# Performance work log

Hardware: AMD Instinct MI355X
Metric: run time of the kernel (lower is better)

The kernel has to match this reference:

```python
import jax, jax.numpy as jnp
import numpy as np

B, L, CIN, C = 256, 65, 2053, 512
SCALE = 1.0 / float(np.sqrt(C))


def _attn_layer(x, Wq, bq, Wk, bk, Wv, bv):
    # x: [B, Cin, L]; Conv1d(kernel=1) == channel-mixing matmul
    q = jnp.einsum('oi,bil->bol', Wq, x) + bq[:, None]
    k = jnp.einsum('oi,bil->bol', Wk, x) + bk[:, None]
    v = jax.nn.leaky_relu(jnp.einsum('oi,bil->bol', Wv, x) + bv[:, None], 0.01)
    # att[b,l,m] = <q[:,l], k[:,m]> / sqrt(C); softmax over m
    att = jax.nn.softmax(jnp.einsum('bcl,bcm->blm', q, k) * SCALE, axis=-1)
    # original: sum_m att[b,l,1,m] * v[b,1,c,m] -> [B,L,C] -> permute -> [B,C,L]
    out = jnp.einsum('blm,bcm->bcl', att, v)
    return out + x if out.shape == x.shape else out  # residual only when channels match


def _transform(x, Wq0, bq0, Wk0, bk0, Wv0, bv0, Wq, bq, Wk, bk, Wv, bv):
    x = _attn_layer(x, Wq0, bq0, Wk0, bk0, Wv0, bv0)
    for n in range(3):  # layers 1..3, C->C with residual
        x = _attn_layer(x, Wq[n], bq[n], Wk[n], bk[n], Wv[n], bv[n])
    return x


def setup_inputs():
    key = jax.random.key(0)
    ks = jax.random.split(key, 20)
    s = 0.02
    inp = {
        'dataleft': jax.random.normal(ks[0], (B, L, CIN), jnp.float32),
        'dataright': jax.random.normal(ks[1], (B, L, CIN), jnp.float32),
        # layer-0 QKV conv1d (k=1) weights: [C, CIN]
        'Wq0': jax.random.normal(ks[2], (C, CIN), jnp.float32) * s,
        'bq0': jnp.zeros((C,), jnp.float32),
        'Wk0': jax.random.normal(ks[3], (C, CIN), jnp.float32) * s,
        'bk0': jnp.zeros((C,), jnp.float32),
        'Wv0': jax.random.normal(ks[4], (C, CIN), jnp.float32) * s,
        'bv0': jnp.zeros((C,), jnp.float32),
        # layers 1..3 stacked: [3, C, C]
        'Wq': jax.random.normal(ks[5], (3, C, C), jnp.float32) * s,
        'bq': jnp.zeros((3, C), jnp.float32),
        'Wk': jax.random.normal(ks[6], (3, C, C), jnp.float32) * s,
        'bk': jnp.zeros((3, C), jnp.float32),
        'Wv': jax.random.normal(ks[7], (3, C, C), jnp.float32) * s,
        'bv': jnp.zeros((3, C), jnp.float32),
        # classifier: fc1(1024->256), fc2(256->2)
        'W1': jax.random.normal(ks[8], (256, 2 * C), jnp.float32) * s,
        'b1': jnp.zeros((256,), jnp.float32),
        'W2': jax.random.normal(ks[9], (2, 256), jnp.float32) * s,
        'b2': jnp.zeros((2,), jnp.float32),
    }
    return inp


def reference(dataleft, dataright, Wq0, bq0, Wk0, bk0, Wv0, bv0,
              Wq, bq, Wk, bk, Wv, bv, W1, b1, W2, b2):
    xl = jnp.transpose(dataleft, (0, 2, 1))   # [B, CIN, L]
    xr = jnp.transpose(dataright, (0, 2, 1))
    xl = _transform(xl, Wq0, bq0, Wk0, bk0, Wv0, bv0, Wq, bq, Wk, bk, Wv, bv)
    xr = _transform(xr, Wq0, bq0, Wk0, bk0, Wv0, bv0, Wq, bq, Wk, bk, Wv, bv)
    # AdaptiveAvgPool2d((512,1)) on [B,512,L]: identity over channel dim, mean over L
    xl = jnp.mean(xl, axis=-1)  # [B, C]
    xr = jnp.mean(xr, axis=-1)
    h = jnp.concatenate([xl, xr], axis=1)            # [B, 2C]
    h = jax.nn.relu(h @ W1.T + b1)                   # [B, 256]
    y = h @ W2.T + b2                                # [B, 2]
    return y  # training mode: no final softmax
```

## Files before the change

kernel.cpp:

```cpp
#include <hip/hip_runtime.h>
#include <hip/hip_bf16.h>

#define BF16 __hip_bfloat16

typedef __bf16 bf16x8 __attribute__((ext_vector_type(8)));
typedef float f32x4 __attribute__((ext_vector_type(4)));

__device__ __forceinline__ void async_copy16(const void* g, void* l) {
    __builtin_amdgcn_global_load_lds(
        (const __attribute__((address_space(1))) void*)g,
        (__attribute__((address_space(3))) void*)l,
        16, 0, 0);
}

__global__ __launch_bounds__(256) void convert_pad_k(
    const float* __restrict__ src, BF16* __restrict__ dst,
    long pairs, int Ks, int Kd) {
    long p = (long)blockIdx.x * blockDim.x + threadIdx.x;
    if (p >= pairs) return;
    long e = p * 2;
    long r = e / Kd;
    int k = (int)(e - r * Kd);
    float a = (k < Ks) ? src[r * Ks + k] : 0.f;
    float b = (k + 1 < Ks) ? src[r * Ks + k + 1] : 0.f;
    dst[e] = __float2bfloat16(a);
    dst[e + 1] = __float2bfloat16(b);
}

__global__ __launch_bounds__(256, 3) void gemm_qkv(
    const BF16* __restrict__ Xg, const BF16* __restrict__ Wg,
    const float* __restrict__ bqp, const float* __restrict__ bkp, const float* __restrict__ bvp,
    BF16* __restrict__ Qo, BF16* __restrict__ Ko, BF16* __restrict__ Vo,
    int K, int vtmode) {
    __shared__ __align__(16) BF16 Xs[2][128 * 32];
    __shared__ __align__(16) BF16 Ws[2][128 * 32];
    const int tid = threadIdx.x;
    const int w = tid >> 6;
    const int lane = tid & 63;
    const int quad = lane >> 4;
    const int l15 = lane & 15;
    const long n0 = (long)blockIdx.y * 128;
    const int m0full = blockIdx.x * 128;
    const int sel = blockIdx.x >> 2;
    const int mbase = (blockIdx.x & 3) * 128;
    const int wn = (w & 1) * 64;
    const int wm = (w >> 1) * 64;
    const int srow = lane >> 2;
    const int skoff = (lane & 3) * 8;
    f32x4 acc[4][4] = {};
    for (int k0 = 0; k0 < K; k0 += 64) {
#pragma unroll
        for (int sub = 0; sub < 2; ++sub) {
#pragma unroll
            for (int c = 0; c < 2; ++c) {
                const int rbase = w * 32 + c * 16;
                const int kcol = k0 + sub * 32 + skoff;
                async_copy16(Xg + (n0 + rbase + srow) * K + kcol, &Xs[sub][rbase * 32]);
                async_copy16(Wg + (long)(m0full + rbase + srow) * K + kcol, &Ws[sub][rbase * 32]);
            }
        }
        __syncthreads();
#pragma unroll
        for (int sub = 0; sub < 2; ++sub) {
            bf16x8 af[4], bfr[4];
#pragma unroll
            for (int i = 0; i < 4; ++i)
                af[i] = *(const bf16x8*)&Xs[sub][(wn + i * 16 + l15) * 32 + quad * 8];
#pragma unroll
            for (int j = 0; j < 4; ++j)
                bfr[j] = *(const bf16x8*)&Ws[sub][(wm + j * 16 + l15) * 32 + quad * 8];
#pragma unroll
            for (int i = 0; i < 4; ++i)
#pragma unroll
                for (int j = 0; j < 4; ++j)
                    acc[i][j] = __builtin_amdgcn_mfma_f32_16x16x32_bf16(af[i], bfr[j], acc[i][j], 0, 0, 0);
        }
        __syncthreads();
    }
    const float* bp = (sel == 0) ? bqp : (sel == 1) ? bkp : bvp;
    BF16* out = (sel == 0) ? Qo : (sel == 1) ? Ko : Vo;
#pragma unroll
    for (int j = 0; j < 4; ++j) {
        const int m = mbase + wm + j * 16 + l15;
        const float bz = bp[m];
#pragma unroll
        for (int i = 0; i < 4; ++i) {
#pragma unroll
            for (int r = 0; r < 4; ++r) {
                const long n = n0 + wn + i * 16 + quad * 4 + r;
                float v = acc[i][j][r] + bz;
                if (sel == 2) {
                    v = (v >= 0.f) ? v : 0.01f * v;
                    if (vtmode) {
                        const int ni = (int)n;
                        const int bb = ni / 65;
                        const int l = ni - bb * 65;
                        out[((long)bb * 512 + m) * 96 + l] = __float2bfloat16(v);
                        continue;
                    }
                }
                out[n * 512 + m] = __float2bfloat16(v);
            }
        }
    }
}

__global__ __launch_bounds__(256) void vtrans_k(const ushort* __restrict__ Vb,
                                                ushort* __restrict__ Vt) {
    const int bb = blockIdx.x;
    for (int idx = threadIdx.x; idx < 512 * 33; idx += 256) {
        const int c = idx / 33;
        const int m = (idx - c * 33) * 2;
        ushort a = Vb[((long)bb * 65 + m) * 512 + c];
        ushort b = (m + 1 < 65) ? Vb[((long)bb * 65 + m + 1) * 512 + c] : (ushort)0;
        *(uint*)&Vt[((long)bb * 512 + c) * 96 + m] = (uint)a | ((uint)b << 16);
    }
}

__global__ __launch_bounds__(256) void attn_scores(
    const BF16* __restrict__ Qg, const BF16* __restrict__ Kg, BF16* __restrict__ Pg) {
    constexpr float SC = 0.04419417382415922f;
    __shared__ __align__(16) BF16 Qs[2][80 * 32];
    __shared__ __align__(16) BF16 Ks[2][80 * 32];
    __shared__ float Sf[80 * 84];
    const int bb = blockIdx.x;
    const int tid = threadIdx.x;
    const int w = tid >> 6, lane = tid & 63, quad = lane >> 4, l15 = lane & 15;
    int i16[7], j16[7], nt = 0;
    for (int t = w; t < 25; t += 4) {
        i16[nt] = (t / 5) * 16;
        j16[nt] = (t % 5) * 16;
        ++nt;
    }
    f32x4 acc[7] = {};
    for (int k0 = 0; k0 < 512; k0 += 64) {
        for (int idx = tid; idx < 1280; idx += 256) {
            const int t = (idx >= 640) ? 1 : 0;
            const int e = idx - t * 640;
            const int sub = (e >= 320) ? 1 : 0;
            const int e2 = e - sub * 320;
            const int row = e2 >> 2;
            const int koff = (e2 & 3) * 8;
            uint4 val = make_uint4(0, 0, 0, 0);
            if (row < 65) {
                const BF16* src = (t ? Kg : Qg) + ((long)(bb * 65 + row) * 512 + k0 + sub * 32 + koff);
                val = *(const uint4*)src;
            }
            *(uint4*)&((t ? Ks : Qs)[sub][row * 32 + koff]) = val;
        }
        __syncthreads();
#pragma unroll
        for (int sub = 0; sub < 2; ++sub) {
            for (int u = 0; u < nt; ++u) {
                bf16x8 af = *(const bf16x8*)&Qs[sub][(i16[u] + l15) * 32 + quad * 8];
                bf16x8 bfr = *(const bf16x8*)&Ks[sub][(j16[u] + l15) * 32 + quad * 8];
                acc[u] = __builtin_amdgcn_mfma_f32_16x16x32_bf16(af, bfr, acc[u], 0, 0, 0);
            }
        }
        __syncthreads();
    }
    for (int u = 0; u < nt; ++u)
#pragma unroll
        for (int r = 0; r < 4; ++r)
            Sf[(i16[u] + quad * 4 + r) * 84 + j16[u] + l15] = acc[u][r] * SC;
    __syncthreads();
    for (int rr = tid >> 2; rr < 65; rr += 64) {
        const int sub = tid & 3;
        float mx = -1e30f;
        for (int m = sub; m < 65; m += 4) mx = fmaxf(mx, Sf[rr * 84 + m]);
        mx = fmaxf(mx, __shfl_xor(mx, 1));
        mx = fmaxf(mx, __shfl_xor(mx, 2));
        float s = 0.f;
        for (int m = sub; m < 65; m += 4) {
            float e = __expf(Sf[rr * 84 + m] - mx);
            Sf[rr * 84 + m] = e;
            s += e;
        }
        s += __shfl_xor(s, 1);
        s += __shfl_xor(s, 2);
        const float inv = 1.f / s;
        const long base = ((long)bb * 65 + rr) * 96;
        for (int m = sub; m < 96; m += 4) {
            float v = (m < 65) ? Sf[rr * 84 + m] * inv : 0.f;
            Pg[base + m] = __float2bfloat16(v);
        }
    }
}

__global__ __launch_bounds__(256) void attn_pv(
    const BF16* __restrict__ Pg, const BF16* __restrict__ Vt,
    BF16* __restrict__ Xg, int residual) {
    __shared__ __align__(16) BF16 Ps[80 * 104];
    const int bb = blockIdx.x;
    const int c0 = blockIdx.y * 128;
    const int tid = threadIdx.x;
    const int w = tid >> 6, lane = tid & 63, quad = lane >> 4, l15 = lane & 15;
    for (int idx = tid; idx < 960; idx += 256) {
        const int row = idx / 12;
        const int kk = idx - row * 12;
        uint4 val = make_uint4(0, 0, 0, 0);
        if (row < 65) val = *(const uint4*)(Pg + ((long)bb * 65 + row) * 96 + kk * 8);
        *(uint4*)&Ps[row * 104 + kk * 8] = val;
    }
    __syncthreads();
    bf16x8 af[5][3];
#pragma unroll
    for (int i = 0; i < 5; ++i)
#pragma unroll
        for (int ks = 0; ks < 3; ++ks)
            af[i][ks] = *(const bf16x8*)&Ps[(i * 16 + l15) * 104 + ks * 32 + quad * 8];
#pragma unroll
    for (int jj = 0; jj < 2; ++jj) {
        const int c = c0 + (jj * 4 + w) * 16 + l15;
        const BF16* vp = Vt + ((long)bb * 512 + c) * 96 + quad * 8;
        bf16x8 b0 = *(const bf16x8*)vp;
        bf16x8 b1 = *(const bf16x8*)(vp + 32);
        bf16x8 b2 = *(const bf16x8*)(vp + 64);
        f32x4 po[5] = {};
#pragma unroll
        for (int i = 0; i < 5; ++i) {
            po[i] = __builtin_amdgcn_mfma_f32_16x16x32_bf16(af[i][0], b0, po[i], 0, 0, 0);
            po[i] = __builtin_amdgcn_mfma_f32_16x16x32_bf16(af[i][1], b1, po[i], 0, 0, 0);
            po[i] = __builtin_amdgcn_mfma_f32_16x16x32_bf16(af[i][2], b2, po[i], 0, 0, 0);
        }
#pragma unroll
        for (int i = 0; i < 5; ++i)
#pragma unroll
            for (int r = 0; r < 4; ++r) {
                const int l = i * 16 + quad * 4 + r;
                if (l < 65) {
                    const long idx = ((long)(bb * 65 + l)) * 512 + c;
                    float v = po[i][r];
                    if (residual) v += __bfloat162float(Xg[idx]);
                    Xg[idx] = __float2bfloat16(v);
                }
            }
    }
}

__global__ __launch_bounds__(256) void pool_k(const BF16* __restrict__ Xg,
                                              float* __restrict__ Hp) {
    const int sb = blockIdx.x;
    const int s = sb >> 8, b = sb & 255;
    for (int c = threadIdx.x; c < 512; c += 256) {
        float acc = 0.f;
        for (int l = 0; l < 65; ++l)
            acc += __bfloat162float(Xg[((long)sb * 65 + l) * 512 + c]);
        Hp[(long)b * 1024 + s * 512 + c] = acc * (1.f / 65.f);
    }
}

__global__ __launch_bounds__(256) void fc_k(
    const float* __restrict__ Hp, const float* __restrict__ W1,
    const float* __restrict__ b1, const float* __restrict__ W2,
    const float* __restrict__ b2, float* __restrict__ out) {
    __shared__ float h[1024];
    __shared__ float h1[256];
    const int b = blockIdx.x, tid = threadIdx.x;
    for (int k = tid; k < 1024; k += 256) h[k] = Hp[(long)b * 1024 + k];
    __syncthreads();
    float acc = b1[tid];
    for (int k = 0; k < 1024; ++k) acc += W1[(long)tid * 1024 + k] * h[k];
    h1[tid] = fmaxf(acc, 0.f);
    __syncthreads();
    const int w = tid >> 6, lane = tid & 63;
    if (w < 2) {
        float p = 0.f;
        for (int u = lane; u < 256; u += 64) p += W2[w * 256 + u] * h1[u];
        for (int off = 32; off > 0; off >>= 1) p += __shfl_down(p, off);
        if (lane == 0) out[b * 2 + w] = p + b2[w];
    }
}

extern "C" void kernel_launch(void* const* d_in, const int* in_sizes, int n_in,
                              void* d_out, int out_size, void* d_ws, size_t ws_size,
                              hipStream_t stream) {
    const float* dataL = (const float*)d_in[0];
    const float* dataR = (const float*)d_in[1];
    const float* Wq0 = (const float*)d_in[2];
    const float* bq0 = (const float*)d_in[3];
    const float* Wk0 = (const float*)d_in[4];
    const float* bk0 = (const float*)d_in[5];
    const float* Wv0 = (const float*)d_in[6];
    const float* bv0 = (const float*)d_in[7];
    const float* Wq = (const float*)d_in[8];
    const float* bq = (const float*)d_in[9];
    const float* Wk = (const float*)d_in[10];
    const float* bk = (const float*)d_in[11];
    const float* Wv = (const float*)d_in[12];
    const float* bv = (const float*)d_in[13];
    const float* W1 = (const float*)d_in[14];
    const float* b1 = (const float*)d_in[15];
    const float* W2 = (const float*)d_in[16];
    const float* b2 = (const float*)d_in[17];

    char* ws = (char*)d_ws;
    BF16* Xb = (BF16*)ws;
    BF16* X = Xb;
    BF16* Vt = (BF16*)(ws + 34078720L);
    BF16* Pg = (BF16*)(ws + 84410368L);
    float* Hp = (float*)(ws + 90800128L);
    BF16* Wc = (BF16*)(ws + 140574720L);
    BF16* Qb = (BF16*)(ws + 151781376L);
    BF16* Kb = (BF16*)(ws + 185860096L);
    BF16* Vb = (BF16*)(ws + 219938816L);

    BF16* w0 = Wc;
    BF16* wl = Wc + 3L * 512 * 2112;

    auto cvt = [&](const float* src, BF16* dst, long R, int Ks, int Kd) {
        long pairs = R * Kd / 2;
        int blocks = (int)((pairs + 255) / 256);
        convert_pad_k<<<blocks, 256, 0, stream>>>(src, dst, pairs, Ks, Kd);
    };
    cvt(dataL, Xb, 16640, 2053, 2112);
    cvt(dataR, Xb + 16640L * 2112, 16640, 2053, 2112);
    cvt(Wq0, w0, 512, 2053, 2112);
    cvt(Wk0, w0 + 512L * 2112, 512, 2053, 2112);
    cvt(Wv0, w0 + 2L * 512 * 2112, 512, 2053, 2112);
    for (int n = 0; n < 3; ++n) {
        BF16* base = wl + (long)n * 3 * 262144;
        cvt(Wq + (long)n * 262144, base, 512, 512, 512);
        cvt(Wk + (long)n * 262144, base + 262144, 512, 512, 512);
        cvt(Wv + (long)n * 262144, base + 2 * 262144, 512, 512, 512);
    }

    dim3 ggrid(12, 260);
    dim3 pvgrid(512, 4);
    gemm_qkv<<<ggrid, 256, 0, stream>>>(Xb, w0, bq0, bk0, bv0, Qb, Kb, Vb, 2112, 0);
    vtrans_k<<<512, 256, 0, stream>>>((const ushort*)Vb, (ushort*)Vt);
    attn_scores<<<512, 256, 0, stream>>>(Qb, Kb, Pg);
    attn_pv<<<pvgrid, 256, 0, stream>>>(Pg, Vt, X, 0);
    for (int n = 0; n < 3; ++n) {
        gemm_qkv<<<ggrid, 256, 0, stream>>>(X, wl + (long)n * 3 * 262144,
                                            bq + n * 512, bk + n * 512, bv + n * 512,
                                            Qb, Kb, Vt, 512, 1);
        attn_scores<<<512, 256, 0, stream>>>(Qb, Kb, Pg);
        attn_pv<<<pvgrid, 256, 0, stream>>>(Pg, Vt, X, 1);
    }
    pool_k<<<512, 256, 0, stream>>>(X, Hp);
    fc_k<<<256, 256, 0, stream>>>(Hp, W1, b1, W2, b2, (float*)d_out);
}
```

Before: 1.431 ms.

## Restructure QKV GEMM with 256-row tiles, triple-buffered LDS and swizzle

The QKV projection GEMM moves from a 128x128 tile with 256 threads and double-buffered 32-wide K slices to a 256x128 tile with 512 threads, 64-wide K tiles and a 3-stage async LDS pipeline. Loads are issued two tiles ahead, and the loop waits on vmcnt with a raw s_barrier instead of full __syncthreads. LDS uses an XOR swizzle to avoid bank conflicts, MFMA runs at raised priority, and block IDs are remapped across 8 groups for locality. The aim is to hide global-load latency and cut barrier overhead in the dominant GEMM. The cost is much more LDS per block (about 144KB) and so lower occupancy.

```diff
diff --git a/kernel.cpp b/kernel.cpp
--- a/kernel.cpp
+++ b/kernel.cpp
@@ -27,67 +27,103 @@
     dst[e + 1] = __float2bfloat16(b);
 }
 
-__global__ __launch_bounds__(256, 3) void gemm_qkv(
+__global__ __launch_bounds__(512, 2) void gemm_qkv(
     const BF16* __restrict__ Xg, const BF16* __restrict__ Wg,
     const float* __restrict__ bqp, const float* __restrict__ bkp, const float* __restrict__ bvp,
     BF16* __restrict__ Qo, BF16* __restrict__ Ko, BF16* __restrict__ Vo,
     int K, int vtmode) {
-    __shared__ __align__(16) BF16 Xs[2][128 * 32];
-    __shared__ __align__(16) BF16 Ws[2][128 * 32];
+    __shared__ __align__(16) BF16 As[3][256 * 64];
+    __shared__ __align__(16) BF16 Bs[3][128 * 64];
     const int tid = threadIdx.x;
     const int w = tid >> 6;
     const int lane = tid & 63;
     const int quad = lane >> 4;
     const int l15 = lane & 15;
-    const long n0 = (long)blockIdx.y * 128;
-    const int m0full = blockIdx.x * 128;
-    const int sel = blockIdx.x >> 2;
-    const int mbase = (blockIdx.x & 3) * 128;
-    const int wn = (w & 1) * 64;
-    const int wm = (w >> 1) * 64;
-    const int srow = lane >> 2;
-    const int skoff = (lane & 3) * 8;
+    const int linear = blockIdx.x + 12 * blockIdx.y;
+    const int cpx = (12 * (int)gridDim.y) >> 3;
+    const int id2 = (linear & 7) * cpx + (linear >> 3);
+    const int bx = id2 % 12;
+    const int by = id2 / 12;
+    const long n0 = (long)by * 256;
+    const long m0full = (long)bx * 128;
+    const int sel = bx >> 2;
+    const int mbase = (bx & 3) * 128;
+    const int wr = (w >> 1) * 64;
+    const int wc = (w & 1) * 64;
+    const int KT = K >> 6;
+    const int rl = lane >> 3;
+    const int gsw = ((lane & 7) ^ (rl & 7)) * 8;
+    const int rw = w * 8 + rl;
+
+#define STAGE_TILE(k0, buf)                                                              \
+    do {                                                                                 \
+        _Pragma("unroll")                                                                \
+        for (int r_ = 0; r_ < 4; ++r_)                                                   \
+            async_copy16(Xg + (n0 + r_ * 64 + rw) * K + (k0) + gsw,                      \
+                         &As[buf][(r_ * 64 + w * 8) * 64]);                              \
+        _Pragma("unroll")                                                                \
+        for (int r_ = 0; r_ < 2; ++r_)                                                   \
+            async_copy16(Wg + (m0full + r_ * 64 + rw) * K + (k0) + gsw,                  \
+                         &Bs[buf][(r_ * 64 + w * 8) * 64]);                              \
+    } while (0)
+
     f32x4 acc[4][4] = {};
-    for (int k0 = 0; k0 < K; k0 += 64) {
-#pragma unroll
-        for (int sub = 0; sub < 2; ++sub) {
-#pragma unroll
-            for (int c = 0; c < 2; ++c) {
-                const int rbase = w * 32 + c * 16;
-                const int kcol = k0 + sub * 32 + skoff;
-                async_copy16(Xg + (n0 + rbase + srow) * K + kcol, &Xs[sub][rbase * 32]);
-                async_copy16(Wg + (long)(m0full + rbase + srow) * K + kcol, &Ws[sub][rbase * 32]);
-            }
-        }
-        __syncthreads();
-#pragma unroll
-        for (int sub = 0; sub < 2; ++sub) {
-            bf16x8 af[4], bfr[4];
+    STAGE_TILE(0, 0);
+    STAGE_TILE(64, 1);
+    int cb = 0;
+    for (int kt = 0; kt < KT; ++kt) {
+        if (kt + 1 < KT) {
+            asm volatile("s_waitcnt vmcnt(6)\n\ts_barrier" ::: "memory");
+        } else {
+            asm volatile("s_waitcnt vmcnt(0)\n\ts_barrier" ::: "memory");
+        }
+        __builtin_amdgcn_sched_barrier(0);
+        bf16x8 af[2][4], bfr[2][4];
+#pragma unroll
+        for (int s = 0; s < 2; ++s) {
+#pragma unroll
+            for (int i = 0; i < 4; ++i) {
+                const int row = wr + i * 16 + l15;
+                const int gx = ((s * 4 + quad) ^ (row & 7)) * 8;
+                af[s][i] = *(const bf16x8*)&As[cb][row * 64 + gx];
+            }
+#pragma unroll
+            for (int j = 0; j < 4; ++j) {
+                const int row = wc + j * 16 + l15;
+                const int gx = ((s * 4 + quad) ^ (row & 7)) * 8;
+                bfr[s][j] = *(const bf16x8*)&Bs[cb][row * 64 + gx];
+            }
+        }
+        if (kt + 2 < KT) {
+            int nb = cb + 2;
+            if (nb >= 3) nb -= 3;
+            STAGE_TILE((kt + 2) << 6, nb);
+        }
+        __builtin_amdgcn_s_setprio(1);
+#pragma unroll
+        for (int s = 0; s < 2; ++s)
 #pragma unroll
             for (int i = 0; i < 4; ++i)
-                af[i] = *(const bf16x8*)&Xs[sub][(wn + i * 16 + l15) * 32 + quad * 8];
-#pragma unroll
-            for (int j = 0; j < 4; ++j)
-                bfr[j] = *(const bf16x8*)&Ws[sub][(wm + j * 16 + l15) * 32 + quad * 8];
-#pragma unroll
-            for (int i = 0; i < 4; ++i)
 #pragma unroll
                 for (int j = 0; j < 4; ++j)
-                    acc[i][j] = __builtin_amdgcn_mfma_f32_16x16x32_bf16(af[i], bfr[j], acc[i][j], 0, 0, 0);
-        }
-        __syncthreads();
-    }
+                    acc[i][j] = __builtin_amdgcn_mfma_f32_16x16x32_bf16(af[s][i], bfr[s][j], acc[i][j], 0, 0, 0);
+        __builtin_amdgcn_s_setprio(0);
+        ++cb;
+        if (cb >= 3) cb -= 3;
+    }
+#undef STAGE_TILE
+
     const float* bp = (sel == 0) ? bqp : (sel == 1) ? bkp : bvp;
     BF16* out = (sel == 0) ? Qo : (sel == 1) ? Ko : Vo;
 #pragma unroll
     for (int j = 0; j < 4; ++j) {
-        const int m = mbase + wm + j * 16 + l15;
+        const int m = mbase + wc + j * 16 + l15;
         const float bz = bp[m];
 #pragma unroll
         for (int i = 0; i < 4; ++i) {
 #pragma unroll
             for (int r = 0; r < 4; ++r) {
-                const long n = n0 + wn + i * 16 + quad * 4 + r;
+                const long n = n0 + wr + i * 16 + quad * 4 + r;
                 float v = acc[i][j][r] + bz;
                 if (sel == 2) {
                     v = (v >= 0.f) ? v : 0.01f * v;
@@ -325,14 +361,14 @@
         cvt(Wv + (long)n * 262144, base + 2 * 262144, 512, 512, 512);
     }
 
-    dim3 ggrid(12, 260);
+    dim3 ggrid(12, 130);
     dim3 pvgrid(512, 4);
-    gemm_qkv<<<ggrid, 256, 0, stream>>>(Xb, w0, bq0, bk0, bv0, Qb, Kb, Vb, 2112, 0);
+    gemm_qkv<<<ggrid, 512, 0, stream>>>(Xb, w0, bq0, bk0, bv0, Qb, Kb, Vb, 2112, 0);
     vtrans_k<<<512, 256, 0, stream>>>((const ushort*)Vb, (ushort*)Vt);
     attn_scores<<<512, 256, 0, stream>>>(Qb, Kb, Pg);
     attn_pv<<<pvgrid, 256, 0, stream>>>(Pg, Vt, X, 0);
     for (int n = 0; n < 3; ++n) {
-        gemm_qkv<<<ggrid, 256, 0, stream>>>(X, wl + (long)n * 3 * 262144,
+        gemm_qkv<<<ggrid, 512, 0, stream>>>(X, wl + (long)n * 3 * 262144,
                                             bq + n * 512, bk + n * 512, bv + n * 512,
                                             Qb, Kb, Vt, 512, 1);
         attn_scores<<<512, 256, 0, stream>>>(Qb, Kb, Pg);
```

After: 1.338 ms. -6.5%, faster.
